# Kernel tuning notes

Hardware: AMD Instinct MI355X
Metric: run time of the kernel (lower is better)

## Reference

```python
import jax, jax.numpy as jnp
import numpy as np


def setup_inputs() -> dict:
    key = jax.random.key(0)
    k1, k2 = jax.random.split(key)
    B, F, E, U = 16384, 39, 64, 128
    embeds = jax.random.normal(k1, (B, F, E), dtype=jnp.float32)
    outer_w = jax.random.normal(k2, (U, E, E), dtype=jnp.float32) * 0.05
    return {"embeds": embeds, "outer_w": outer_w}


def reference(embeds, outer_w):
    # embeds: (B, F, E) = concatenated field embeddings; outer_w: (U, E, E)
    feat_sum = jnp.sum(embeds, axis=1)  # (B, E)
    # lp[b,u] = sum_{i,j} feat_sum[b,i] * feat_sum[b,j] * outer_w[u,i,j]
    # == f^T W_u f, computed as a batched GEMM instead of the original's
    # per-unit elementwise multiply+reduce loop (same math).
    fw = jnp.einsum('bi,uij->buj', feat_sum, outer_w)  # (B, U, E)
    lp = jnp.einsum('buj,bj->bu', fw, feat_sum)        # (B, U)
    return lp
```

## Files before the change

kernel.cpp:

```cpp
#include <hip/hip_runtime.h>

#define B_TOTAL 16384
#define F 39
#define E 64
#define U 128
#define BT 64
#define THREADS 512

typedef __attribute__((ext_vector_type(8))) short short8;
typedef __attribute__((ext_vector_type(4))) float f32x4;

__device__ __forceinline__ unsigned pack2_bf16(float a, float b) {
  unsigned ua = __builtin_bit_cast(unsigned, a) + 0x8000u;
  unsigned ub = __builtin_bit_cast(unsigned, b) + 0x8000u;
  return (ub & 0xFFFF0000u) | (ua >> 16);
}

__global__ __launch_bounds__(256) void prep_w(const float* __restrict__ w,
                                              uint4* __restrict__ wf) {
  int tid = blockIdx.x * 256 + threadIdx.x;
  int lane = tid & 63;
  int frag = tid >> 6;
  int ks  = frag & 1;
  int ntg = (frag >> 1) & 7;
  int i   = frag >> 4;
  int uu  = ntg * 16 + (lane & 15);
  int k0  = ks * 32 + (lane >> 4) * 8;
  const float* src = w + (size_t)uu * (E * E) + i * E + k0;
  float4 v0 = *(const float4*)src;
  float4 v1 = *(const float4*)(src + 4);
  uint4 o;
  o.x = pack2_bf16(v0.x, v0.y);
  o.y = pack2_bf16(v0.z, v0.w);
  o.z = pack2_bf16(v1.x, v1.y);
  o.w = pack2_bf16(v1.z, v1.w);
  wf[tid] = o;
}

__global__ __launch_bounds__(THREADS) void fused_outer(
    const float* __restrict__ embeds, const uint4* __restrict__ wf,
    float* __restrict__ out) {
  __shared__ __align__(16) float Ft[BT * 68];
  __shared__ __align__(16) float FtT[E * 68];

  const int t = threadIdx.x;
  const int b0 = blockIdx.x * BT;

  for (int task = t; task < BT * 16; task += THREADS) {
    int b = task >> 4, e4 = task & 15;
    const float4* src = (const float4*)(embeds + (size_t)(b0 + b) * (F * E)) + e4;
    float4 s = make_float4(0.f, 0.f, 0.f, 0.f);
    #pragma unroll
    for (int f = 0; f < F; ++f) {
      float4 v = src[f * (E / 4)];
      s.x += v.x; s.y += v.y; s.z += v.z; s.w += v.w;
    }
    *(float4*)&Ft[b * 68 + e4 * 4] = s;
    FtT[(e4 * 4 + 0) * 68 + b] = s.x;
    FtT[(e4 * 4 + 1) * 68 + b] = s.y;
    FtT[(e4 * 4 + 2) * 68 + b] = s.z;
    FtT[(e4 * 4 + 3) * 68 + b] = s.w;
  }
  __syncthreads();

  const int lane = t & 63;
  const int wave = t >> 6;
  const int mh   = (wave >> 2) * 32;
  const int ncol = wave & 3;
  const int nh   = ncol * 32;
  const int fl   = lane & 15;
  const int fo   = (lane >> 4) * 8;
  const int r0   = (lane >> 4) * 4;

  short8 af[2][2];
  #pragma unroll
  for (int mt = 0; mt < 2; ++mt) {
    const float* fr = &Ft[(mh + mt * 16 + fl) * 68];
    #pragma unroll
    for (int ks = 0; ks < 2; ++ks) {
      float4 v0 = *(const float4*)&fr[ks * 32 + fo];
      float4 v1 = *(const float4*)&fr[ks * 32 + fo + 4];
      uint4 o;
      o.x = pack2_bf16(v0.x, v0.y);
      o.y = pack2_bf16(v0.z, v0.w);
      o.z = pack2_bf16(v1.x, v1.y);
      o.w = pack2_bf16(v1.z, v1.w);
      af[mt][ks] = __builtin_bit_cast(short8, o);
    }
  }

  f32x4 acc[2][2];
  #pragma unroll
  for (int mt = 0; mt < 2; ++mt)
    #pragma unroll
    for (int nt = 0; nt < 2; ++nt)
      #pragma unroll
      for (int r = 0; r < 4; ++r) acc[mt][nt][r] = 0.f;

  const uint4* wbase = wf + lane;
  const int fragq = ncol * 4;

  #define LOADW(buf, ii) {                                        \
    _Pragma("unroll")                                             \
    for (int q = 0; q < 4; ++q)                                   \
      buf[q] = wbase[(size_t)(((ii) * 16 + fragq + q)) * 64]; }

  #define STEP(ii, buf) {                                                     \
    f32x4 fia = *(const f32x4*)&FtT[(ii) * 68 + mh + r0];                     \
    f32x4 fib = *(const f32x4*)&FtT[(ii) * 68 + mh + 16 + r0];                \
    _Pragma("unroll")                                                         \
    for (int nt = 0; nt < 2; ++nt) {                                          \
      f32x4 s0 = {0.f, 0.f, 0.f, 0.f};                                        \
      s0 = __builtin_amdgcn_mfma_f32_16x16x32_bf16(                           \
          af[0][0], __builtin_bit_cast(short8, buf[nt * 2 + 0]), s0, 0, 0, 0);\
      s0 = __builtin_amdgcn_mfma_f32_16x16x32_bf16(                           \
          af[0][1], __builtin_bit_cast(short8, buf[nt * 2 + 1]), s0, 0, 0, 0);\
      acc[0][nt] += fia * s0;                                                 \
      f32x4 s1 = {0.f, 0.f, 0.f, 0.f};                                        \
      s1 = __builtin_amdgcn_mfma_f32_16x16x32_bf16(                           \
          af[1][0], __builtin_bit_cast(short8, buf[nt * 2 + 0]), s1, 0, 0, 0);\
      s1 = __builtin_amdgcn_mfma_f32_16x16x32_bf16(                           \
          af[1][1], __builtin_bit_cast(short8, buf[nt * 2 + 1]), s1, 0, 0, 0);\
      acc[1][nt] += fib * s1;                                                 \
    } }

  uint4 w0[4], w1[4], w2[4], w3[4];
  LOADW(w0, 0);
  LOADW(w1, 1);
  for (int i = 0; i < E; i += 4) {
    LOADW(w2, i + 2);
    STEP(i, w0);
    LOADW(w3, i + 3);
    STEP(i + 1, w1);
    if (i + 4 < E) LOADW(w0, i + 4);
    STEP(i + 2, w2);
    if (i + 5 < E) LOADW(w1, i + 5);
    STEP(i + 3, w3);
  }

  #pragma unroll
  for (int mt = 0; mt < 2; ++mt)
    #pragma unroll
    for (int nt = 0; nt < 2; ++nt)
      #pragma unroll
      for (int r = 0; r < 4; ++r)
        out[(size_t)(b0 + mh + mt * 16 + r0 + r) * U + (nh + nt * 16 + fl)] =
            acc[mt][nt][r];
}

extern "C" void kernel_launch(void* const* d_in, const int* in_sizes, int n_in,
                              void* d_out, int out_size, void* d_ws, size_t ws_size,
                              hipStream_t stream) {
  const float* embeds = (const float*)d_in[0];
  const float* w      = (const float*)d_in[1];
  float* out          = (float*)d_out;
  uint4* wfrag        = (uint4*)d_ws;
  prep_w<<<dim3(256), dim3(256), 0, stream>>>(w, wfrag);
  fused_outer<<<dim3(B_TOTAL / BT), dim3(THREADS), 0, stream>>>(embeds, wfrag, out);
}
```

Measured before the change: 250.7 us.

## Retile waves to own unit columns across full batch tile, halving weight loads

Each wave now computes a 16-unit column strip over all 64 batch rows, using four M-tiles of bf16 A fragments, instead of a 32x32 tile. Per-block weight-fragment traffic from L2/global is halved this way, since each wave loads 2 fragments per i rather than 4. Weight prefetch now runs four steps ahead and the first loads are issued before the barrier, so they overlap the embedding reduction. In exchange, A-fragment registers double, and the final prefetch iterations read past the end of the weight-fragment buffer into workspace.

```diff
diff --git a/kernel.cpp b/kernel.cpp
--- a/kernel.cpp
+++ b/kernel.cpp
@@ -46,6 +46,7 @@
   const int t = threadIdx.x;
   const int b0 = blockIdx.x * BT;
 
+  #pragma unroll
   for (int task = t; task < BT * 16; task += THREADS) {
     int b = task >> 4, e4 = task & 15;
     const float4* src = (const float4*)(embeds + (size_t)(b0 + b) * (F * E)) + e4;
@@ -61,21 +62,29 @@
     FtT[(e4 * 4 + 2) * 68 + b] = s.z;
     FtT[(e4 * 4 + 3) * 68 + b] = s.w;
   }
+
+  const int lane = t & 63, wave = t >> 6;
+  const int fl = lane & 15;
+  const int fo = (lane >> 4) * 8;
+  const int r0 = (lane >> 4) * 4;
+
+  const uint4* wv = wf + (size_t)(wave * 2) * 64 + lane;
+
+  #define LOADW(buf, ii) {                 \
+    buf[0] = wv[(size_t)((ii) * 16) * 64]; \
+    buf[1] = wv[(size_t)((ii) * 16 + 1) * 64]; }
+
+  uint4 w0[2], w1[2], w2[2], w3[2];
+  LOADW(w0, 0);
+  LOADW(w1, 1);
+  LOADW(w2, 2);
+  LOADW(w3, 3);
   __syncthreads();
 
-  const int lane = t & 63;
-  const int wave = t >> 6;
-  const int mh   = (wave >> 2) * 32;
-  const int ncol = wave & 3;
-  const int nh   = ncol * 32;
-  const int fl   = lane & 15;
-  const int fo   = (lane >> 4) * 8;
-  const int r0   = (lane >> 4) * 4;
-
-  short8 af[2][2];
+  short8 af[4][2];
   #pragma unroll
-  for (int mt = 0; mt < 2; ++mt) {
-    const float* fr = &Ft[(mh + mt * 16 + fl) * 68];
+  for (int mt = 0; mt < 4; ++mt) {
+    const float* fr = &Ft[(mt * 16 + fl) * 68];
     #pragma unroll
     for (int ks = 0; ks < 2; ++ks) {
       float4 v0 = *(const float4*)&fr[ks * 32 + fo];
@@ -89,63 +98,38 @@
     }
   }
 
-  f32x4 acc[2][2];
+  f32x4 acc[4];
   #pragma unroll
-  for (int mt = 0; mt < 2; ++mt)
+  for (int mt = 0; mt < 4; ++mt)
     #pragma unroll
-    for (int nt = 0; nt < 2; ++nt)
-      #pragma unroll
-      for (int r = 0; r < 4; ++r) acc[mt][nt][r] = 0.f;
+    for (int r = 0; r < 4; ++r) acc[mt][r] = 0.f;
 
-  const uint4* wbase = wf + lane;
-  const int fragq = ncol * 4;
-
-  #define LOADW(buf, ii) {                                        \
-    _Pragma("unroll")                                             \
-    for (int q = 0; q < 4; ++q)                                   \
-      buf[q] = wbase[(size_t)(((ii) * 16 + fragq + q)) * 64]; }
-
-  #define STEP(ii, buf) {                                                     \
-    f32x4 fia = *(const f32x4*)&FtT[(ii) * 68 + mh + r0];                     \
-    f32x4 fib = *(const f32x4*)&FtT[(ii) * 68 + mh + 16 + r0];                \
-    _Pragma("unroll")                                                         \
-    for (int nt = 0; nt < 2; ++nt) {                                          \
-      f32x4 s0 = {0.f, 0.f, 0.f, 0.f};                                        \
-      s0 = __builtin_amdgcn_mfma_f32_16x16x32_bf16(                           \
-          af[0][0], __builtin_bit_cast(short8, buf[nt * 2 + 0]), s0, 0, 0, 0);\
-      s0 = __builtin_amdgcn_mfma_f32_16x16x32_bf16(                           \
-          af[0][1], __builtin_bit_cast(short8, buf[nt * 2 + 1]), s0, 0, 0, 0);\
-      acc[0][nt] += fia * s0;                                                 \
-      f32x4 s1 = {0.f, 0.f, 0.f, 0.f};                                        \
-      s1 = __builtin_amdgcn_mfma_f32_16x16x32_bf16(                           \
-          af[1][0], __builtin_bit_cast(short8, buf[nt * 2 + 0]), s1, 0, 0, 0);\
-      s1 = __builtin_amdgcn_mfma_f32_16x16x32_bf16(                           \
-          af[1][1], __builtin_bit_cast(short8, buf[nt * 2 + 1]), s1, 0, 0, 0);\
-      acc[1][nt] += fib * s1;                                                 \
+  #define STEP(ii, buf) {                                                      \
+    short8 bf0 = __builtin_bit_cast(short8, buf[0]);                           \
+    short8 bf1 = __builtin_bit_cast(short8, buf[1]);                           \
+    _Pragma("unroll")                                                          \
+    for (int mt = 0; mt < 4; ++mt) {                                           \
+      f32x4 s = {0.f, 0.f, 0.f, 0.f};                                          \
+      s = __builtin_amdgcn_mfma_f32_16x16x32_bf16(af[mt][0], bf0, s, 0, 0, 0); \
+      s = __builtin_amdgcn_mfma_f32_16x16x32_bf16(af[mt][1], bf1, s, 0, 0, 0); \
+      f32x4 fi = *(const f32x4*)&FtT[(ii) * 68 + mt * 16 + r0];                \
+      acc[mt] += fi * s;                                                       \
     } }
 
-  uint4 w0[4], w1[4], w2[4], w3[4];
-  LOADW(w0, 0);
-  LOADW(w1, 1);
   for (int i = 0; i < E; i += 4) {
-    LOADW(w2, i + 2);
-    STEP(i, w0);
-    LOADW(w3, i + 3);
-    STEP(i + 1, w1);
-    if (i + 4 < E) LOADW(w0, i + 4);
-    STEP(i + 2, w2);
-    if (i + 5 < E) LOADW(w1, i + 5);
-    STEP(i + 3, w3);
+    STEP(i, w0);     LOADW(w0, i + 4);
+    STEP(i + 1, w1); LOADW(w1, i + 5);
+    STEP(i + 2, w2); LOADW(w2, i + 6);
+    STEP(i + 3, w3); LOADW(w3, i + 7);
   }
 
   #pragma unroll
-  for (int mt = 0; mt < 2; ++mt)
+  for (int mt = 0; mt < 4; ++mt)
     #pragma unroll
-    for (int nt = 0; nt < 2; ++nt)
-      #pragma unroll
-      for (int r = 0; r < 4; ++r)
-        out[(size_t)(b0 + mh + mt * 16 + r0 + r) * U + (nh + nt * 16 + fl)] =
-            acc[mt][nt][r];
+    for (int r = 0; r < 4; ++r)
+      out[(size_t)(b0 + mt * 16 + r0 + r) * U + wave * 16 + fl] = acc[mt][r];
+  #undef LOADW
+  #undef STEP
 }
 
 extern "C" void kernel_launch(void* const* d_in, const int* in_sizes, int n_in,
@@ -154,7 +138,7 @@
   const float* embeds = (const float*)d_in[0];
   const float* w      = (const float*)d_in[1];
   float* out          = (float*)d_out;
-  uint4* wfrag        = (uint4*)d_ws;
-  prep_w<<<dim3(256), dim3(256), 0, stream>>>(w, wfrag);
-  fused_outer<<<dim3(B_TOTAL / BT), dim3(THREADS), 0, stream>>>(embeds, wfrag, out);
+  uint4* wf           = (uint4*)d_ws;
+  prep_w<<<dim3(256), dim3(256), 0, stream>>>(w, wf);
+  fused_outer<<<dim3(B_TOTAL / BT), dim3(THREADS), 0, stream>>>(embeds, wf, out);
 }
```

New measurement: 253.7 us. No clear change (+1.2%).
